# Kernel optimization log

Hardware: AMD Instinct MI355X
Metric: run time of the kernel (lower is better)

## Reference

```python
import jax, jax.numpy as jnp
import numpy as np

NEG_SLOPE = 0.2  # PyG GATConv default leaky_relu slope


def gat_conv(x, src, dst, n, W, a_src, a_dst, bias, concat):
    """PyG-style GATConv (add_self_loops already applied to src/dst)."""
    H, C = a_src.shape
    h = (x @ W).reshape(n, H, C)                      # [N,H,C]
    al_src = jnp.einsum('nhc,hc->nh', h, a_src)       # [N,H]
    al_dst = jnp.einsum('nhc,hc->nh', h, a_dst)       # [N,H]
    e = jax.nn.leaky_relu(al_src[src] + al_dst[dst], NEG_SLOPE)  # [E,H]
    # segment softmax over incoming edges of each dst node
    m = jax.ops.segment_max(e, dst, num_segments=n)   # [N,H]
    ex = jnp.exp(e - m[dst])
    denom = jax.ops.segment_sum(ex, dst, num_segments=n)
    alpha = ex / denom[dst]                            # [E,H]
    out = jax.ops.segment_sum(h[src] * alpha[:, :, None], dst, num_segments=n)  # [N,H,C]
    if concat:
        out = out.reshape(n, H * C)
    else:
        out = out.mean(axis=1)
    return out + bias


def setup_inputs() -> dict:
    key = jax.random.key(0)
    ks = jax.random.split(key, 12)
    N, E = 100000, 1600000
    IN, HID, OUT, H = 128, 16, 32, 4
    x = jax.random.normal(ks[0], (N, IN), dtype=jnp.float32)
    edge_index = jax.random.randint(ks[1], (2, E), 0, N, dtype=jnp.int64)
    s = 0.1
    W1 = jax.random.normal(ks[2], (IN, H * HID), dtype=jnp.float32) * s
    a_src1 = jax.random.normal(ks[3], (H, HID), dtype=jnp.float32) * s
    a_dst1 = jax.random.normal(ks[4], (H, HID), dtype=jnp.float32) * s
    b1 = jnp.zeros((H * HID,), dtype=jnp.float32)
    W2 = jax.random.normal(ks[5], (H * HID, H * OUT), dtype=jnp.float32) * s
    a_src2 = jax.random.normal(ks[6], (H, OUT), dtype=jnp.float32) * s
    a_dst2 = jax.random.normal(ks[7], (H, OUT), dtype=jnp.float32) * s
    b2 = jnp.zeros((OUT,), dtype=jnp.float32)
    return {"x": x, "edge_index": edge_index,
            "W1": W1, "a_src1": a_src1, "a_dst1": a_dst1, "b1": b1,
            "W2": W2, "a_src2": a_src2, "a_dst2": a_dst2, "b2": b2}


def reference(x, edge_index, W1, a_src1, a_dst1, b1, W2, a_src2, a_dst2, b2):
    n = x.shape[0]
    loop = jnp.arange(n, dtype=edge_index.dtype)
    src = jnp.concatenate([edge_index[0], loop])
    dst = jnp.concatenate([edge_index[1], loop])
    # dropout is identity at inference
    h = gat_conv(x, src, dst, n, W1, a_src1, a_dst1, b1, concat=True)
    h = gat_conv(h, src, dst, n, W2, a_src2, a_dst2, b2, concat=False)
    h = jax.nn.elu(h)
    return jax.nn.log_softmax(h, axis=1)
```

## Files before the change

### kernel.cpp

```cpp
#include <hip/hip_runtime.h>
#include <hip/hip_fp16.h>
#include <cstdint>
#include <cstddef>

#define NEG 0.2f
#define TILE 4096


__global__ __launch_bounds__(256) void hist_k(const int* __restrict__ ei, int* __restrict__ cnt, int E) {
    int i = blockIdx.x * 256 + threadIdx.x;
    if (i < E) atomicAdd(&cnt[__builtin_nontemporal_load(ei + E + i)], 1);
}

__global__ __launch_bounds__(256) void scan1_k(const int* __restrict__ cnt, int* __restrict__ rp,
                                               int* __restrict__ bs, int N) {
    __shared__ int sm[256];
    int t = threadIdx.x, i = blockIdx.x * 256 + t;
    int v = (i < N) ? cnt[i] : 0;
    sm[t] = v; __syncthreads();
    for (int off = 1; off < 256; off <<= 1) {
        int u = (t >= off) ? sm[t - off] : 0;
        __syncthreads();
        sm[t] += u;
        __syncthreads();
    }
    if (i < N) rp[i] = sm[t] - v;
    if (t == 255) bs[blockIdx.x] = sm[255];
}

__global__ __launch_bounds__(1024) void scan2_k(int* __restrict__ bs, int nb) {
    __shared__ int sm[1024];
    int t = threadIdx.x;
    int v = (t < nb) ? bs[t] : 0;
    sm[t] = v; __syncthreads();
    for (int off = 1; off < 1024; off <<= 1) {
        int u = (t >= off) ? sm[t - off] : 0;
        __syncthreads();
        sm[t] += u;
        __syncthreads();
    }
    if (t < nb) bs[t] = sm[t] - v;
}

__global__ __launch_bounds__(256) void scan3_k(int* __restrict__ rp, const int* __restrict__ bs, int N) {
    int i = blockIdx.x * 256 + threadIdx.x;
    if (i < N) rp[i] += bs[blockIdx.x];
}

__global__ __launch_bounds__(256) void initA_k(const int* __restrict__ rp, int* __restrict__ curA, int nbk) {
    int b = threadIdx.x;
    if (b < nbk) curA[b] = rp[b << 9];
}


__global__ __launch_bounds__(256) void partA_k(const int* __restrict__ ei, int* __restrict__ curA,
                                               uint2* __restrict__ pairs, int E, int nbk) {
    __shared__ int scnt[256];
    __shared__ int sc[256];
    __shared__ int sbase[256];
    __shared__ int gbase[256];
    __shared__ int cur2[256];
    __shared__ int ssrc[TILE];
    __shared__ int sdst[TILE];
    int t = threadIdx.x;
    int ntiles = (E + TILE - 1) / TILE;
    for (int tile = blockIdx.x; tile < ntiles; tile += gridDim.x) {
        int base = tile * TILE;
        int cntE = min(TILE, E - base);
        scnt[t] = 0;
        __syncthreads();
        int mys[16], myd[16];
        #pragma unroll
        for (int j = 0; j < 16; j++) {
            int i = base + t + 256 * j;
            int s = 0, d = -1;
            if (i < E) {
                s = __builtin_nontemporal_load(ei + i);
                d = __builtin_nontemporal_load(ei + E + i);
            }
            mys[j] = s; myd[j] = d;
            if (d >= 0) atomicAdd(&scnt[d >> 9], 1);
        }
        __syncthreads();
        sc[t] = scnt[t];
        __syncthreads();
        for (int off = 1; off < 256; off <<= 1) {
            int u = (t >= off) ? sc[t - off] : 0;
            __syncthreads();
            sc[t] += u;
            __syncthreads();
        }
        int myb = sc[t] - scnt[t];
        sbase[t] = myb;
        cur2[t] = myb;
        if (t < nbk && scnt[t] > 0) gbase[t] = atomicAdd(&curA[t], scnt[t]);
        __syncthreads();
        #pragma unroll
        for (int j = 0; j < 16; j++) {
            int d = myd[j];
            if (d >= 0) {
                int b = d >> 9;
                int pos = atomicAdd(&cur2[b], 1);
                ssrc[pos] = mys[j];
                sdst[pos] = d;
            }
        }
        __syncthreads();
        for (int i = t; i < cntE; i += 256) {
            int d = sdst[i];
            int b = d >> 9;
            int addr = gbase[b] + (i - sbase[b]);
            pairs[addr] = make_uint2((unsigned)ssrc[i], (unsigned)d);
        }
        __syncthreads();
    }
}


__global__ __launch_bounds__(256) void partB_pairs_k(const uint2* __restrict__ pin, const int* __restrict__ rp,
                                                     int* __restrict__ srcout, int E, int N) {
    __shared__ int cur[512];
    int b = blockIdx.x;
    int t = threadIdx.x;
    int d0 = b << 9;
    cur[t] = 0; cur[t + 256] = 0;
    __syncthreads();
    int hi = d0 + 512;
    int ebase = rp[d0];
    int eend = (hi >= N) ? E : rp[hi];
    for (int j = ebase + t; j < eend; j += 256) {
        uint2 p = pin[j];
        int d = (int)p.y;
        int pos = rp[d] + atomicAdd(&cur[d - d0], 1);
        srcout[pos] = (int)p.x;
    }
}


__global__ __launch_bounds__(256) void gemm1_k(const float* __restrict__ x, const float* __restrict__ W,
                                               const float* __restrict__ a_src, const float* __restrict__ a_dst,
                                               __half* __restrict__ h, float* __restrict__ alsrc,
                                               float* __restrict__ aldst, int N) {
    __shared__ float Bs[128 * 64];
    __shared__ float xs[64][68];
    int t = threadIdx.x;
    for (int i = t; i < 128 * 64 / 4; i += 256)
        ((float4*)Bs)[i] = ((const float4*)W)[i];
    int ct = t & 15, rt = t >> 4;
    int head = ct >> 2, cq = ct & 3;
    float asv[4], adv[4];
    #pragma unroll
    for (int j = 0; j < 4; j++) {
        asv[j] = a_src[head * 16 + 4 * cq + j];
        adv[j] = a_dst[head * 16 + 4 * cq + j];
    }
    int ntiles = (N + 63) >> 6;
    for (int tile = blockIdx.x; tile < ntiles; tile += gridDim.x) {
        int r0 = tile << 6;
        float acc[4][4];
        #pragma unroll
        for (int i = 0; i < 4; i++)
            #pragma unroll
            for (int j = 0; j < 4; j++) acc[i][j] = 0.f;
        for (int kc = 0; kc < 128; kc += 64) {
            __syncthreads();
            int srow = t >> 4, sf4 = t & 15;
            #pragma unroll
            for (int p = 0; p < 4; p++) {
                int r = r0 + srow + 16 * p;
                float4 v = make_float4(0.f, 0.f, 0.f, 0.f);
                if (r < N) v = *(const float4*)(x + (size_t)r * 128 + kc + 4 * sf4);
                *(float4*)&xs[srow + 16 * p][4 * sf4] = v;
            }
            __syncthreads();
            #pragma unroll 4
            for (int k = 0; k < 64; k++) {
                float4 bv = *(float4*)&Bs[(kc + k) * 64 + 4 * ct];
                #pragma unroll
                for (int i = 0; i < 4; i++) {
                    float xv = xs[4 * rt + i][k];
                    acc[i][0] = fmaf(xv, bv.x, acc[i][0]);
                    acc[i][1] = fmaf(xv, bv.y, acc[i][1]);
                    acc[i][2] = fmaf(xv, bv.z, acc[i][2]);
                    acc[i][3] = fmaf(xv, bv.w, acc[i][3]);
                }
            }
        }
        #pragma unroll
        for (int i = 0; i < 4; i++) {
            int r = r0 + 4 * rt + i;
            float ps = 0.f, pd = 0.f;
            #pragma unroll
            for (int j = 0; j < 4; j++) {
                ps = fmaf(acc[i][j], asv[j], ps);
                pd = fmaf(acc[i][j], adv[j], pd);
            }
            ps += __shfl_xor(ps, 1); ps += __shfl_xor(ps, 2);
            pd += __shfl_xor(pd, 1); pd += __shfl_xor(pd, 2);
            if (r < N) {
                __half2 h0 = __floats2half2_rn(acc[i][0], acc[i][1]);
                __half2 h1 = __floats2half2_rn(acc[i][2], acc[i][3]);
                *(__half2*)(h + (size_t)r * 64 + 4 * ct) = h0;
                *(__half2*)(h + (size_t)r * 64 + 4 * ct + 2) = h1;
                if (cq == 0) { alsrc[r * 4 + head] = ps; aldst[r * 4 + head] = pd; }
            }
        }
    }
}


__global__ __launch_bounds__(256) void node1_k(const __half* __restrict__ h, const int* __restrict__ srccol,
                                               const float* __restrict__ alsrc, const float* __restrict__ aldst,
                                               const int* __restrict__ rp, const int* __restrict__ cnt,
                                               const float* __restrict__ bias, __half* __restrict__ out, int N) {
    int t = threadIdx.x;
    int d = (blockIdx.x * 256 + t) >> 4;
    if (d >= N) return;
    int c = t & 15;
    int hc = c >> 2;
    const __half2* hb = (const __half2*)h;
    unsigned co = 2u * c;
    float ad = aldst[d * 4 + hc];
    float e = alsrc[d * 4 + hc] + ad;
    float w = __expf(e > 0.f ? e : NEG * e);
    float den = w;
    __half2 wp = __float2half2_rn(w);
    uint2 u = *(const uint2*)(hb + ((unsigned)d << 5) + co);
    __half2 acc0 = __hmul2(wp, *(__half2*)&u.x);
    __half2 acc1 = __hmul2(wp, *(__half2*)&u.y);
    int start = rp[d], deg = cnt[d];
    int i = 0;
    for (; i + 3 < deg; i += 4) {
        int s0 = srccol[start + i];
        int s1 = srccol[start + i + 1];
        int s2 = srccol[start + i + 2];
        int s3 = srccol[start + i + 3];
        uint2 u0 = *(const uint2*)(hb + ((unsigned)s0 << 5) + co);
        uint2 u1 = *(const uint2*)(hb + ((unsigned)s1 << 5) + co);
        uint2 u2 = *(const uint2*)(hb + ((unsigned)s2 << 5) + co);
        uint2 u3 = *(const uint2*)(hb + ((unsigned)s3 << 5) + co);
        float e0 = alsrc[s0 * 4 + hc] + ad;
        float e1 = alsrc[s1 * 4 + hc] + ad;
        float e2 = alsrc[s2 * 4 + hc] + ad;
        float e3 = alsrc[s3 * 4 + hc] + ad;
        float w0 = __expf(e0 > 0.f ? e0 : NEG * e0);
        float w1 = __expf(e1 > 0.f ? e1 : NEG * e1);
        float w2 = __expf(e2 > 0.f ? e2 : NEG * e2);
        float w3 = __expf(e3 > 0.f ? e3 : NEG * e3);
        den += (w0 + w1) + (w2 + w3);
        __half2 p0 = __float2half2_rn(w0), p1 = __float2half2_rn(w1);
        __half2 p2 = __float2half2_rn(w2), p3 = __float2half2_rn(w3);
        acc0 = __hfma2(p0, *(__half2*)&u0.x, acc0);
        acc1 = __hfma2(p0, *(__half2*)&u0.y, acc1);
        acc0 = __hfma2(p1, *(__half2*)&u1.x, acc0);
        acc1 = __hfma2(p1, *(__half2*)&u1.y, acc1);
        acc0 = __hfma2(p2, *(__half2*)&u2.x, acc0);
        acc1 = __hfma2(p2, *(__half2*)&u2.y, acc1);
        acc0 = __hfma2(p3, *(__half2*)&u3.x, acc0);
        acc1 = __hfma2(p3, *(__half2*)&u3.y, acc1);
    }
    for (; i < deg; i++) {
        int s = srccol[start + i];
        uint2 us = *(const uint2*)(hb + ((unsigned)s << 5) + co);
        float es = alsrc[s * 4 + hc] + ad;
        float ws = __expf(es > 0.f ? es : NEG * es);
        den += ws;
        __half2 wps = __float2half2_rn(ws);
        acc0 = __hfma2(wps, *(__half2*)&us.x, acc0);
        acc1 = __hfma2(wps, *(__half2*)&us.y, acc1);
    }
    float inv = 1.f / den;
    float2 f0 = __half22float2(acc0), f1 = __half22float2(acc1);
    float4 b = *(const float4*)(bias + 4 * c);
    __half2 o0 = __floats2half2_rn(f0.x * inv + b.x, f0.y * inv + b.y);
    __half2 o1 = __floats2half2_rn(f1.x * inv + b.z, f1.y * inv + b.w);
    uint2 o; o.x = *(unsigned*)&o0; o.y = *(unsigned*)&o1;
    *(uint2*)(out + (size_t)d * 64 + 4 * c) = o;
}


__global__ __launch_bounds__(256) void gemm2_k(const __half* __restrict__ xh, const float* __restrict__ W,
                                               const float* __restrict__ a_src, const float* __restrict__ a_dst,
                                               __half* __restrict__ h, float* __restrict__ alsrc,
                                               float* __restrict__ aldst, int N) {
    __shared__ float Bs[64 * 128];
    __shared__ float xs[64][68];
    int t = threadIdx.x;
    for (int i = t; i < 64 * 128 / 4; i += 256)
        ((float4*)Bs)[i] = ((const float4*)W)[i];
    int ct = t & 15, rt = t >> 4;
    int hA = ct >> 3, cq = ct & 7;
    float asA[4], adA[4], asB[4], adB[4];
    #pragma unroll
    for (int j = 0; j < 4; j++) {
        asA[j] = a_src[hA * 32 + 4 * cq + j];
        adA[j] = a_dst[hA * 32 + 4 * cq + j];
        asB[j] = a_src[(2 + hA) * 32 + 4 * cq + j];
        adB[j] = a_dst[(2 + hA) * 32 + 4 * cq + j];
    }
    int ntiles = (N + 63) >> 6;
    for (int tile = blockIdx.x; tile < ntiles; tile += gridDim.x) {
        int r0 = tile << 6;
        float accA[4][4], accB[4][4];
        #pragma unroll
        for (int i = 0; i < 4; i++)
            #pragma unroll
            for (int j = 0; j < 4; j++) { accA[i][j] = 0.f; accB[i][j] = 0.f; }
        __syncthreads();
        int srow = t >> 3, su = t & 7;
        #pragma unroll
        for (int p = 0; p < 2; p++) {
            int r = r0 + srow + 32 * p;
            float2 g0 = make_float2(0.f, 0.f), g1 = g0, g2 = g0, g3 = g0;
            if (r < N) {
                uint4 u = *(const uint4*)(xh + (size_t)r * 64 + 8 * su);
                const __half2* hp = (const __half2*)&u;
                g0 = __half22float2(hp[0]); g1 = __half22float2(hp[1]);
                g2 = __half22float2(hp[2]); g3 = __half22float2(hp[3]);
            }
            *(float4*)&xs[srow + 32 * p][8 * su] = make_float4(g0.x, g0.y, g1.x, g1.y);
            *(float4*)&xs[srow + 32 * p][8 * su + 4] = make_float4(g2.x, g2.y, g3.x, g3.y);
        }
        __syncthreads();
        #pragma unroll 4
        for (int k = 0; k < 64; k++) {
            float4 bA = *(float4*)&Bs[k * 128 + 4 * ct];
            float4 bB = *(float4*)&Bs[k * 128 + 64 + 4 * ct];
            #pragma unroll
            for (int i = 0; i < 4; i++) {
                float xv = xs[4 * rt + i][k];
                accA[i][0] = fmaf(xv, bA.x, accA[i][0]);
                accA[i][1] = fmaf(xv, bA.y, accA[i][1]);
                accA[i][2] = fmaf(xv, bA.z, accA[i][2]);
                accA[i][3] = fmaf(xv, bA.w, accA[i][3]);
                accB[i][0] = fmaf(xv, bB.x, accB[i][0]);
                accB[i][1] = fmaf(xv, bB.y, accB[i][1]);
                accB[i][2] = fmaf(xv, bB.z, accB[i][2]);
                accB[i][3] = fmaf(xv, bB.w, accB[i][3]);
            }
        }
        #pragma unroll
        for (int i = 0; i < 4; i++) {
            int r = r0 + 4 * rt + i;
            float psA = 0.f, pdA = 0.f, psB = 0.f, pdB = 0.f;
            #pragma unroll
            for (int j = 0; j < 4; j++) {
                psA = fmaf(accA[i][j], asA[j], psA);
                pdA = fmaf(accA[i][j], adA[j], pdA);
                psB = fmaf(accB[i][j], asB[j], psB);
                pdB = fmaf(accB[i][j], adB[j], pdB);
            }
            #pragma unroll
            for (int off = 1; off <= 4; off <<= 1) {
                psA += __shfl_xor(psA, off); pdA += __shfl_xor(pdA, off);
                psB += __shfl_xor(psB, off); pdB += __shfl_xor(pdB, off);
            }
            if (r < N) {
                __half2 hA0 = __floats2half2_rn(accA[i][0], accA[i][1]);
                __half2 hA1 = __floats2half2_rn(accA[i][2], accA[i][3]);
                __half2 hB0 = __floats2half2_rn(accB[i][0], accB[i][1]);
                __half2 hB1 = __floats2half2_rn(accB[i][2], accB[i][3]);
                *(__half2*)(h + (size_t)r * 128 + 4 * ct) = hA0;
                *(__half2*)(h + (size_t)r * 128 + 4 * ct + 2) = hA1;
                *(__half2*)(h + (size_t)r * 128 + 64 + 4 * ct) = hB0;
                *(__half2*)(h + (size_t)r * 128 + 64 + 4 * ct + 2) = hB1;
                if (cq == 0) {
                    alsrc[r * 4 + hA] = psA;     alsrc[r * 4 + 2 + hA] = psB;
                    aldst[r * 4 + hA] = pdA;     aldst[r * 4 + 2 + hA] = pdB;
                }
            }
        }
    }
}


__global__ __launch_bounds__(256) void node2_k(const __half* __restrict__ h, const int* __restrict__ srccol,
                                               const float* __restrict__ alsrc, const float* __restrict__ aldst,
                                               const int* __restrict__ rp, const int* __restrict__ cnt,
                                               const float* __restrict__ bias, float* __restrict__ out, int N) {
    int t = threadIdx.x;
    int d = (blockIdx.x * 256 + t) >> 4;
    if (d >= N) return;
    int c = t & 15;
    int hc = c >> 2, jc = c & 3;
    const __half2* hb = (const __half2*)h;
    unsigned co = 4u * c;
    float ad = aldst[d * 4 + hc];
    float e = alsrc[d * 4 + hc] + ad;
    float w = __expf(e > 0.f ? e : NEG * e);
    float den = w;
    __half2 wp = __float2half2_rn(w);
    uint4 u = *(const uint4*)(hb + ((unsigned)d << 6) + co);
    const __half2* hp = (const __half2*)&u;
    __half2 acc[4];
    #pragma unroll
    for (int j = 0; j < 4; j++) acc[j] = __hmul2(wp, hp[j]);
    int start = rp[d], deg = cnt[d];
    int i = 0;
    for (; i + 3 < deg; i += 4) {
        int s0 = srccol[start + i];
        int s1 = srccol[start + i + 1];
        int s2 = srccol[start + i + 2];
        int s3 = srccol[start + i + 3];
        uint4 u0 = *(const uint4*)(hb + ((unsigned)s0 << 6) + co);
        uint4 u1 = *(const uint4*)(hb + ((unsigned)s1 << 6) + co);
        uint4 u2 = *(const uint4*)(hb + ((unsigned)s2 << 6) + co);
        uint4 u3 = *(const uint4*)(hb + ((unsigned)s3 << 6) + co);
        float e0 = alsrc[s0 * 4 + hc] + ad;
        float e1 = alsrc[s1 * 4 + hc] + ad;
        float e2 = alsrc[s2 * 4 + hc] + ad;
        float e3 = alsrc[s3 * 4 + hc] + ad;
        float w0 = __expf(e0 > 0.f ? e0 : NEG * e0);
        float w1 = __expf(e1 > 0.f ? e1 : NEG * e1);
        float w2 = __expf(e2 > 0.f ? e2 : NEG * e2);
        float w3 = __expf(e3 > 0.f ? e3 : NEG * e3);
        den += (w0 + w1) + (w2 + w3);
        __half2 p0 = __float2half2_rn(w0), p1 = __float2half2_rn(w1);
        __half2 p2 = __float2half2_rn(w2), p3 = __float2half2_rn(w3);
        const __half2* q0 = (const __half2*)&u0;
        const __half2* q1 = (const __half2*)&u1;
        const __half2* q2 = (const __half2*)&u2;
        const __half2* q3 = (const __half2*)&u3;
        #pragma unroll
        for (int j = 0; j < 4; j++) acc[j] = __hfma2(p0, q0[j], acc[j]);
        #pragma unroll
        for (int j = 0; j < 4; j++) acc[j] = __hfma2(p1, q1[j], acc[j]);
        #pragma unroll
        for (int j = 0; j < 4; j++) acc[j] = __hfma2(p2, q2[j], acc[j]);
        #pragma unroll
        for (int j = 0; j < 4; j++) acc[j] = __hfma2(p3, q3[j], acc[j]);
    }
    for (; i < deg; i++) {
        int s = srccol[start + i];
        uint4 us = *(const uint4*)(hb + ((unsigned)s << 6) + co);
        float es = alsrc[s * 4 + hc] + ad;
        float ws = __expf(es > 0.f ? es : NEG * es);
        den += ws;
        __half2 wps = __float2half2_rn(ws);
        const __half2* hps = (const __half2*)&us;
        #pragma unroll
        for (int j = 0; j < 4; j++) acc[j] = __hfma2(wps, hps[j], acc[j]);
    }
    float inv = 1.f / den;
    float v[8];
    #pragma unroll
    for (int j = 0; j < 4; j++) {
        float2 f = __half22float2(acc[j]);
        v[2 * j] = f.x * inv; v[2 * j + 1] = f.y * inv;
    }
    #pragma unroll
    for (int off = 4; off <= 8; off <<= 1) {
        #pragma unroll
        for (int j = 0; j < 8; j++) v[j] += __shfl_xor(v[j], off);
    }
    float ev[8];
    #pragma unroll
    for (int j = 0; j < 8; j++) {
        float val = 0.25f * v[j] + bias[8 * jc + j];
        ev[j] = val > 0.f ? val : __expf(val) - 1.f;
    }
    float mx = ev[0];
    #pragma unroll
    for (int j = 1; j < 8; j++) mx = fmaxf(mx, ev[j]);
    #pragma unroll
    for (int off = 1; off <= 2; off <<= 1) mx = fmaxf(mx, __shfl_xor(mx, off));
    float sum = 0.f;
    #pragma unroll
    for (int j = 0; j < 8; j++) sum += __expf(ev[j] - mx);
    #pragma unroll
    for (int off = 1; off <= 2; off <<= 1) sum += __shfl_xor(sum, off);
    float ls = mx + __logf(sum);
    if (c < 4) {
        float4 o0, o1;
        o0.x = ev[0] - ls; o0.y = ev[1] - ls; o0.z = ev[2] - ls; o0.w = ev[3] - ls;
        o1.x = ev[4] - ls; o1.y = ev[5] - ls; o1.z = ev[6] - ls; o1.w = ev[7] - ls;
        *(float4*)(out + (size_t)d * 32 + 8 * jc) = o0;
        *(float4*)(out + (size_t)d * 32 + 8 * jc + 4) = o1;
    }
}


extern "C" void kernel_launch(void* const* d_in, const int* in_sizes, int n_in,
                              void* d_out, int out_size, void* d_ws, size_t ws_size,
                              hipStream_t stream) {
    const float* x   = (const float*)d_in[0];
    const int*   ei  = (const int*)d_in[1];
    const float* W1  = (const float*)d_in[2];
    const float* as1 = (const float*)d_in[3];
    const float* ad1 = (const float*)d_in[4];
    const float* b1  = (const float*)d_in[5];
    const float* W2  = (const float*)d_in[6];
    const float* as2 = (const float*)d_in[7];
    const float* ad2 = (const float*)d_in[8];
    const float* b2  = (const float*)d_in[9];
    float* out = (float*)d_out;
    int N = in_sizes[0] / 128;
    int E = in_sizes[1] / 2;

    char* base = (char*)d_ws;
    size_t off = 0;
    auto alloc = [&](size_t bytes) -> char* {
        char* p = base + off;
        off = (off + bytes + 255) & ~(size_t)255;
        return p;
    };
    __half* h1h   = (__half*)alloc((size_t)N * 64 * 2);
    __half* h1o   = (__half*)alloc((size_t)N * 64 * 2);
    __half* h2h   = (__half*)alloc((size_t)N * 128 * 2);
    float* alsrc1 = (float*)alloc((size_t)N * 4 * 4);
    float* aldst1 = (float*)alloc((size_t)N * 4 * 4);
    float* alsrc2 = (float*)alloc((size_t)N * 4 * 4);
    float* aldst2 = (float*)alloc((size_t)N * 4 * 4);
    int* cnt  = (int*)alloc((size_t)N * 4);
    int* rp   = (int*)alloc((size_t)N * 4);
    int* curA = (int*)alloc(256 * 4);
    int* bs   = (int*)alloc(1024 * 4);
    int* srccol = (int*)alloc((size_t)E * 4);
    uint2* pairs = (uint2*)alloc((size_t)E * 8);

    int nbk = (N + 511) >> 9;
    int ntilesA = (E + TILE - 1) / TILE;
    int nb = (N + 255) / 256;

    hipMemsetAsync(cnt, 0, (size_t)N * 4, stream);
    hist_k<<<(E + 255) / 256, 256, 0, stream>>>(ei, cnt, E);
    scan1_k<<<nb, 256, 0, stream>>>(cnt, rp, bs, N);
    scan2_k<<<1, 1024, 0, stream>>>(bs, nb);
    scan3_k<<<nb, 256, 0, stream>>>(rp, bs, N);
    initA_k<<<1, 256, 0, stream>>>(rp, curA, nbk);
    partA_k<<<ntilesA, 256, 0, stream>>>(ei, curA, pairs, E, nbk);
    partB_pairs_k<<<nbk, 256, 0, stream>>>(pairs, rp, srccol, E, N);

    gemm1_k<<<768, 256, 0, stream>>>(x, W1, as1, ad1, h1h, alsrc1, aldst1, N);
    node1_k<<<(N + 15) / 16, 256, 0, stream>>>(h1h, srccol, alsrc1, aldst1, rp, cnt, b1, h1o, N);
    gemm2_k<<<768, 256, 0, stream>>>(h1o, W2, as2, ad2, h2h, alsrc2, aldst2, N);
    node2_k<<<(N + 15) / 16, 256, 0, stream>>>(h2h, srccol, alsrc2, aldst2, rp, cnt, b2, out, N);
}
```

Before: 384.9 us.

## Reorder layer-2 GAT to aggregate before projection using precomputed attention vectors

Layer 2 now folds the attention vectors into W2 (W2·a_src and W2·a_dst, precomputed in a small kernel), so the attention logits come straight from the 64-wide layer-1 output. The edge gather then reads the 64-wide h1o instead of the 128-wide projected features. It keeps per-head aggregates in a 256-wide fp16 buffer, and a final GEMM applies W2 per head, adds the bias and fuses the head mean, ELU and log_softmax. The goal is to halve gather traffic in the edge-heavy aggregation, at the cost of a larger intermediate write and read and a bigger GEMM. That intermediate buffer reuses the workspace that previously held h1h and pairs.

```diff
diff --git a/kernel.cpp b/kernel.cpp
--- a/kernel.cpp
+++ b/kernel.cpp
@@ -279,122 +279,94 @@
 }
 
 
-__global__ __launch_bounds__(256) void gemm2_k(const __half* __restrict__ xh, const float* __restrict__ W,
-                                               const float* __restrict__ a_src, const float* __restrict__ a_dst,
-                                               __half* __restrict__ h, float* __restrict__ alsrc,
-                                               float* __restrict__ aldst, int N) {
-    __shared__ float Bs[64 * 128];
-    __shared__ float xs[64][68];
-    int t = threadIdx.x;
-    for (int i = t; i < 64 * 128 / 4; i += 256)
-        ((float4*)Bs)[i] = ((const float4*)W)[i];
-    int ct = t & 15, rt = t >> 4;
-    int hA = ct >> 3, cq = ct & 7;
-    float asA[4], adA[4], asB[4], adB[4];
-    #pragma unroll
-    for (int j = 0; j < 4; j++) {
-        asA[j] = a_src[hA * 32 + 4 * cq + j];
-        adA[j] = a_dst[hA * 32 + 4 * cq + j];
-        asB[j] = a_src[(2 + hA) * 32 + 4 * cq + j];
-        adB[j] = a_dst[(2 + hA) * 32 + 4 * cq + j];
-    }
-    int ntiles = (N + 63) >> 6;
-    for (int tile = blockIdx.x; tile < ntiles; tile += gridDim.x) {
-        int r0 = tile << 6;
-        float accA[4][4], accB[4][4];
-        #pragma unroll
-        for (int i = 0; i < 4; i++)
-            #pragma unroll
-            for (int j = 0; j < 4; j++) { accA[i][j] = 0.f; accB[i][j] = 0.f; }
-        __syncthreads();
-        int srow = t >> 3, su = t & 7;
-        #pragma unroll
-        for (int p = 0; p < 2; p++) {
-            int r = r0 + srow + 32 * p;
-            float2 g0 = make_float2(0.f, 0.f), g1 = g0, g2 = g0, g3 = g0;
-            if (r < N) {
-                uint4 u = *(const uint4*)(xh + (size_t)r * 64 + 8 * su);
-                const __half2* hp = (const __half2*)&u;
-                g0 = __half22float2(hp[0]); g1 = __half22float2(hp[1]);
-                g2 = __half22float2(hp[2]); g3 = __half22float2(hp[3]);
-            }
-            *(float4*)&xs[srow + 32 * p][8 * su] = make_float4(g0.x, g0.y, g1.x, g1.y);
-            *(float4*)&xs[srow + 32 * p][8 * su + 4] = make_float4(g2.x, g2.y, g3.x, g3.y);
-        }
-        __syncthreads();
-        #pragma unroll 4
-        for (int k = 0; k < 64; k++) {
-            float4 bA = *(float4*)&Bs[k * 128 + 4 * ct];
-            float4 bB = *(float4*)&Bs[k * 128 + 64 + 4 * ct];
-            #pragma unroll
-            for (int i = 0; i < 4; i++) {
-                float xv = xs[4 * rt + i][k];
-                accA[i][0] = fmaf(xv, bA.x, accA[i][0]);
-                accA[i][1] = fmaf(xv, bA.y, accA[i][1]);
-                accA[i][2] = fmaf(xv, bA.z, accA[i][2]);
-                accA[i][3] = fmaf(xv, bA.w, accA[i][3]);
-                accB[i][0] = fmaf(xv, bB.x, accB[i][0]);
-                accB[i][1] = fmaf(xv, bB.y, accB[i][1]);
-                accB[i][2] = fmaf(xv, bB.z, accB[i][2]);
-                accB[i][3] = fmaf(xv, bB.w, accB[i][3]);
-            }
-        }
-        #pragma unroll
-        for (int i = 0; i < 4; i++) {
-            int r = r0 + 4 * rt + i;
-            float psA = 0.f, pdA = 0.f, psB = 0.f, pdB = 0.f;
-            #pragma unroll
-            for (int j = 0; j < 4; j++) {
-                psA = fmaf(accA[i][j], asA[j], psA);
-                pdA = fmaf(accA[i][j], adA[j], pdA);
-                psB = fmaf(accB[i][j], asB[j], psB);
-                pdB = fmaf(accB[i][j], adB[j], pdB);
-            }
-            #pragma unroll
-            for (int off = 1; off <= 4; off <<= 1) {
-                psA += __shfl_xor(psA, off); pdA += __shfl_xor(pdA, off);
-                psB += __shfl_xor(psB, off); pdB += __shfl_xor(pdB, off);
-            }
-            if (r < N) {
-                __half2 hA0 = __floats2half2_rn(accA[i][0], accA[i][1]);
-                __half2 hA1 = __floats2half2_rn(accA[i][2], accA[i][3]);
-                __half2 hB0 = __floats2half2_rn(accB[i][0], accB[i][1]);
-                __half2 hB1 = __floats2half2_rn(accB[i][2], accB[i][3]);
-                *(__half2*)(h + (size_t)r * 128 + 4 * ct) = hA0;
-                *(__half2*)(h + (size_t)r * 128 + 4 * ct + 2) = hA1;
-                *(__half2*)(h + (size_t)r * 128 + 64 + 4 * ct) = hB0;
-                *(__half2*)(h + (size_t)r * 128 + 64 + 4 * ct + 2) = hB1;
-                if (cq == 0) {
-                    alsrc[r * 4 + hA] = psA;     alsrc[r * 4 + 2 + hA] = psB;
-                    aldst[r * 4 + hA] = pdA;     aldst[r * 4 + 2 + hA] = pdB;
-                }
-            }
-        }
-    }
-}
-
-
-__global__ __launch_bounds__(256) void node2_k(const __half* __restrict__ h, const int* __restrict__ srccol,
-                                               const float* __restrict__ alsrc, const float* __restrict__ aldst,
-                                               const int* __restrict__ rp, const int* __restrict__ cnt,
-                                               const float* __restrict__ bias, float* __restrict__ out, int N) {
+__global__ __launch_bounds__(256) void prew_k(const float* __restrict__ W2, const float* __restrict__ as2,
+                                              const float* __restrict__ ad2, float* __restrict__ was,
+                                              float* __restrict__ wad) {
+    int t = threadIdx.x;
+    int k = t >> 2, hh = t & 3;
+    const float* wrow = W2 + k * 128 + hh * 32;
+    const float* av = as2 + hh * 32;
+    const float* dv = ad2 + hh * 32;
+    float s = 0.f, ds = 0.f;
+    #pragma unroll 8
+    for (int c = 0; c < 32; c++) {
+        float w = wrow[c];
+        s = fmaf(w, av[c], s);
+        ds = fmaf(w, dv[c], ds);
+    }
+    was[t] = s;
+    wad[t] = ds;
+}
+
+
+__global__ __launch_bounds__(256) void alv2_k(const __half* __restrict__ h1o, const float* __restrict__ was,
+                                              const float* __restrict__ wad, float* __restrict__ alsrc,
+                                              float* __restrict__ aldst, int N) {
     int t = threadIdx.x;
     int d = (blockIdx.x * 256 + t) >> 4;
     if (d >= N) return;
     int c = t & 15;
-    int hc = c >> 2, jc = c & 3;
-    const __half2* hb = (const __half2*)h;
-    unsigned co = 4u * c;
-    float ad = aldst[d * 4 + hc];
-    float e = alsrc[d * 4 + hc] + ad;
+    uint2 u = *(const uint2*)(h1o + (size_t)d * 64 + 4 * c);
+    float2 f0 = __half22float2(*(__half2*)&u.x);
+    float2 f1 = __half22float2(*(__half2*)&u.y);
+    float v0 = f0.x, v1 = f0.y, v2 = f1.x, v3 = f1.y;
+    const float4* was4 = (const float4*)was;
+    const float4* wad4 = (const float4*)wad;
+    float4 wa0 = was4[4 * c + 0], wa1 = was4[4 * c + 1], wa2 = was4[4 * c + 2], wa3 = was4[4 * c + 3];
+    float4 wd0 = wad4[4 * c + 0], wd1 = wad4[4 * c + 1], wd2 = wad4[4 * c + 2], wd3 = wad4[4 * c + 3];
+    float4 ps, pd;
+    ps.x = fmaf(v0, wa0.x, fmaf(v1, wa1.x, fmaf(v2, wa2.x, v3 * wa3.x)));
+    ps.y = fmaf(v0, wa0.y, fmaf(v1, wa1.y, fmaf(v2, wa2.y, v3 * wa3.y)));
+    ps.z = fmaf(v0, wa0.z, fmaf(v1, wa1.z, fmaf(v2, wa2.z, v3 * wa3.z)));
+    ps.w = fmaf(v0, wa0.w, fmaf(v1, wa1.w, fmaf(v2, wa2.w, v3 * wa3.w)));
+    pd.x = fmaf(v0, wd0.x, fmaf(v1, wd1.x, fmaf(v2, wd2.x, v3 * wd3.x)));
+    pd.y = fmaf(v0, wd0.y, fmaf(v1, wd1.y, fmaf(v2, wd2.y, v3 * wd3.y)));
+    pd.z = fmaf(v0, wd0.z, fmaf(v1, wd1.z, fmaf(v2, wd2.z, v3 * wd3.z)));
+    pd.w = fmaf(v0, wd0.w, fmaf(v1, wd1.w, fmaf(v2, wd2.w, v3 * wd3.w)));
+    #pragma unroll
+    for (int off = 1; off <= 8; off <<= 1) {
+        ps.x += __shfl_xor(ps.x, off); ps.y += __shfl_xor(ps.y, off);
+        ps.z += __shfl_xor(ps.z, off); ps.w += __shfl_xor(ps.w, off);
+        pd.x += __shfl_xor(pd.x, off); pd.y += __shfl_xor(pd.y, off);
+        pd.z += __shfl_xor(pd.z, off); pd.w += __shfl_xor(pd.w, off);
+    }
+    if (c == 0) {
+        *(float4*)(alsrc + (size_t)d * 4) = ps;
+        *(float4*)(aldst + (size_t)d * 4) = pd;
+    }
+}
+
+
+#define ACC8(P, A, B) { const __half2* qa = (const __half2*)&(A); const __half2* qb = (const __half2*)&(B); \
+    acc0 = __hfma2(P, qa[0], acc0); acc1 = __hfma2(P, qa[1], acc1); \
+    acc2 = __hfma2(P, qa[2], acc2); acc3 = __hfma2(P, qa[3], acc3); \
+    acc4 = __hfma2(P, qb[0], acc4); acc5 = __hfma2(P, qb[1], acc5); \
+    acc6 = __hfma2(P, qb[2], acc6); acc7 = __hfma2(P, qb[3], acc7); }
+
+__global__ __launch_bounds__(256) void node2_k(const __half* __restrict__ h1o, const int* __restrict__ srccol,
+                                               const float* __restrict__ alsrc, const float* __restrict__ aldst,
+                                               const int* __restrict__ rp, const int* __restrict__ cnt,
+                                               __half* __restrict__ y, int N) {
+    int t = threadIdx.x;
+    int d = (blockIdx.x * 256 + t) >> 4;
+    if (d >= N) return;
+    int c = t & 15;
+    int h = c >> 2;
+    unsigned co = 2u * (unsigned)(c & 3);
+    const uint4* hb = (const uint4*)h1o;
+    float ad = aldst[d * 4 + h];
+    float e = alsrc[d * 4 + h] + ad;
     float w = __expf(e > 0.f ? e : NEG * e);
     float den = w;
     __half2 wp = __float2half2_rn(w);
-    uint4 u = *(const uint4*)(hb + ((unsigned)d << 6) + co);
-    const __half2* hp = (const __half2*)&u;
-    __half2 acc[4];
-    #pragma unroll
-    for (int j = 0; j < 4; j++) acc[j] = __hmul2(wp, hp[j]);
+    uint4 ua = hb[((unsigned)d << 3) + co];
+    uint4 ub = hb[((unsigned)d << 3) + co + 1];
+    const __half2* pa = (const __half2*)&ua;
+    const __half2* pb = (const __half2*)&ub;
+    __half2 acc0 = __hmul2(wp, pa[0]), acc1 = __hmul2(wp, pa[1]);
+    __half2 acc2 = __hmul2(wp, pa[2]), acc3 = __hmul2(wp, pa[3]);
+    __half2 acc4 = __hmul2(wp, pb[0]), acc5 = __hmul2(wp, pb[1]);
+    __half2 acc6 = __hmul2(wp, pb[2]), acc7 = __hmul2(wp, pb[3]);
     int start = rp[d], deg = cnt[d];
     int i = 0;
     for (; i + 3 < deg; i += 4) {
@@ -402,14 +374,14 @@
         int s1 = srccol[start + i + 1];
         int s2 = srccol[start + i + 2];
         int s3 = srccol[start + i + 3];
-        uint4 u0 = *(const uint4*)(hb + ((unsigned)s0 << 6) + co);
-        uint4 u1 = *(const uint4*)(hb + ((unsigned)s1 << 6) + co);
-        uint4 u2 = *(const uint4*)(hb + ((unsigned)s2 << 6) + co);
-        uint4 u3 = *(const uint4*)(hb + ((unsigned)s3 << 6) + co);
-        float e0 = alsrc[s0 * 4 + hc] + ad;
-        float e1 = alsrc[s1 * 4 + hc] + ad;
-        float e2 = alsrc[s2 * 4 + hc] + ad;
-        float e3 = alsrc[s3 * 4 + hc] + ad;
+        uint4 a0 = hb[((unsigned)s0 << 3) + co], b0 = hb[((unsigned)s0 << 3) + co + 1];
+        uint4 a1 = hb[((unsigned)s1 << 3) + co], b1 = hb[((unsigned)s1 << 3) + co + 1];
+        uint4 a2 = hb[((unsigned)s2 << 3) + co], b2 = hb[((unsigned)s2 << 3) + co + 1];
+        uint4 a3 = hb[((unsigned)s3 << 3) + co], b3 = hb[((unsigned)s3 << 3) + co + 1];
+        float e0 = alsrc[s0 * 4 + h] + ad;
+        float e1 = alsrc[s1 * 4 + h] + ad;
+        float e2 = alsrc[s2 * 4 + h] + ad;
+        float e3 = alsrc[s3 * 4 + h] + ad;
         float w0 = __expf(e0 > 0.f ? e0 : NEG * e0);
         float w1 = __expf(e1 > 0.f ? e1 : NEG * e1);
         float w2 = __expf(e2 > 0.f ? e2 : NEG * e2);
@@ -417,65 +389,109 @@
         den += (w0 + w1) + (w2 + w3);
         __half2 p0 = __float2half2_rn(w0), p1 = __float2half2_rn(w1);
         __half2 p2 = __float2half2_rn(w2), p3 = __float2half2_rn(w3);
-        const __half2* q0 = (const __half2*)&u0;
-        const __half2* q1 = (const __half2*)&u1;
-        const __half2* q2 = (const __half2*)&u2;
-        const __half2* q3 = (const __half2*)&u3;
-        #pragma unroll
-        for (int j = 0; j < 4; j++) acc[j] = __hfma2(p0, q0[j], acc[j]);
-        #pragma unroll
-        for (int j = 0; j < 4; j++) acc[j] = __hfma2(p1, q1[j], acc[j]);
-        #pragma unroll
-        for (int j = 0; j < 4; j++) acc[j] = __hfma2(p2, q2[j], acc[j]);
-        #pragma unroll
-        for (int j = 0; j < 4; j++) acc[j] = __hfma2(p3, q3[j], acc[j]);
+        ACC8(p0, a0, b0)
+        ACC8(p1, a1, b1)
+        ACC8(p2, a2, b2)
+        ACC8(p3, a3, b3)
     }
     for (; i < deg; i++) {
         int s = srccol[start + i];
-        uint4 us = *(const uint4*)(hb + ((unsigned)s << 6) + co);
-        float es = alsrc[s * 4 + hc] + ad;
+        uint4 as = hb[((unsigned)s << 3) + co], bs = hb[((unsigned)s << 3) + co + 1];
+        float es = alsrc[s * 4 + h] + ad;
         float ws = __expf(es > 0.f ? es : NEG * es);
         den += ws;
-        __half2 wps = __float2half2_rn(ws);
-        const __half2* hps = (const __half2*)&us;
+        __half2 pws = __float2half2_rn(ws);
+        ACC8(pws, as, bs)
+    }
+    float inv = 0.25f / den;
+    __half2 ip = __float2half2_rn(inv);
+    uint4 oA, oB;
+    __half2* oa = (__half2*)&oA; __half2* ob = (__half2*)&oB;
+    oa[0] = __hmul2(ip, acc0); oa[1] = __hmul2(ip, acc1);
+    oa[2] = __hmul2(ip, acc2); oa[3] = __hmul2(ip, acc3);
+    ob[0] = __hmul2(ip, acc4); ob[1] = __hmul2(ip, acc5);
+    ob[2] = __hmul2(ip, acc6); ob[3] = __hmul2(ip, acc7);
+    __half* yp = y + (size_t)d * 256 + 16u * (unsigned)c;
+    *(uint4*)yp = oA;
+    *(uint4*)(yp + 8) = oB;
+}
+
+
+__global__ __launch_bounds__(256) void gemm3_k(const __half* __restrict__ y, const float* __restrict__ W2,
+                                               const float* __restrict__ bias, float* __restrict__ out, int N) {
+    __shared__ __half2 ws[256 * 16];
+    __shared__ __half2 ys[64 * 134];
+    int t = threadIdx.x;
+    for (int i = t; i < 4096; i += 256) {
+        int kp = i >> 4, c2 = i & 15;
+        int hh = kp >> 6, kk = kp & 63;
+        const float* wp = W2 + kk * 128 + hh * 32 + 2 * c2;
+        ws[i] = __floats2half2_rn(wp[0], wp[1]);
+    }
+    int ct = t & 7, rt = t >> 3;
+    float4 b4 = *(const float4*)(bias + 4 * ct);
+    int ntiles = (N + 63) >> 6;
+    for (int tile = blockIdx.x; tile < ntiles; tile += gridDim.x) {
+        int r0 = tile << 6;
+        __syncthreads();
+        for (int i = t; i < 64 * 64; i += 256) {
+            int row = i >> 6, k4 = i & 63;
+            uint2 v = make_uint2(0u, 0u);
+            int r = r0 + row;
+            if (r < N) v = *(const uint2*)(y + (size_t)r * 256 + 4 * k4);
+            *(uint2*)&ys[row * 134 + 2 * k4] = v;
+        }
+        __syncthreads();
+        float acc[2][4];
         #pragma unroll
-        for (int j = 0; j < 4; j++) acc[j] = __hfma2(wps, hps[j], acc[j]);
-    }
-    float inv = 1.f / den;
-    float v[8];
-    #pragma unroll
-    for (int j = 0; j < 4; j++) {
-        float2 f = __half22float2(acc[j]);
-        v[2 * j] = f.x * inv; v[2 * j + 1] = f.y * inv;
-    }
-    #pragma unroll
-    for (int off = 4; off <= 8; off <<= 1) {
+        for (int r = 0; r < 2; r++)
+            #pragma unroll
+            for (int j = 0; j < 4; j++) acc[r][j] = 0.f;
+        const __half2* yr0 = ys + (2 * rt) * 134;
+        const __half2* yr1 = ys + (2 * rt + 1) * 134;
+        #pragma unroll 4
+        for (int k2 = 0; k2 < 128; k2++) {
+            const __half2* wk0 = ws + (2 * k2) * 16;
+            const __half2* wk1 = wk0 + 16;
+            float2 wA0 = __half22float2(wk0[2 * ct]);
+            float2 wA1 = __half22float2(wk0[2 * ct + 1]);
+            float2 wB0 = __half22float2(wk1[2 * ct]);
+            float2 wB1 = __half22float2(wk1[2 * ct + 1]);
+            float2 xa = __half22float2(yr0[k2]);
+            float2 xb = __half22float2(yr1[k2]);
+            acc[0][0] = fmaf(xa.x, wA0.x, acc[0][0]); acc[0][1] = fmaf(xa.x, wA0.y, acc[0][1]);
+            acc[0][2] = fmaf(xa.x, wA1.x, acc[0][2]); acc[0][3] = fmaf(xa.x, wA1.y, acc[0][3]);
+            acc[0][0] = fmaf(xa.y, wB0.x, acc[0][0]); acc[0][1] = fmaf(xa.y, wB0.y, acc[0][1]);
+            acc[0][2] = fmaf(xa.y, wB1.x, acc[0][2]); acc[0][3] = fmaf(xa.y, wB1.y, acc[0][3]);
+            acc[1][0] = fmaf(xb.x, wA0.x, acc[1][0]); acc[1][1] = fmaf(xb.x, wA0.y, acc[1][1]);
+            acc[1][2] = fmaf(xb.x, wA1.x, acc[1][2]); acc[1][3] = fmaf(xb.x, wA1.y, acc[1][3]);
+            acc[1][0] = fmaf(xb.y, wB0.x, acc[1][0]); acc[1][1] = fmaf(xb.y, wB0.y, acc[1][1]);
+            acc[1][2] = fmaf(xb.y, wB1.x, acc[1][2]); acc[1][3] = fmaf(xb.y, wB1.y, acc[1][3]);
+        }
         #pragma unroll
-        for (int j = 0; j < 8; j++) v[j] += __shfl_xor(v[j], off);
-    }
-    float ev[8];
-    #pragma unroll
-    for (int j = 0; j < 8; j++) {
-        float val = 0.25f * v[j] + bias[8 * jc + j];
-        ev[j] = val > 0.f ? val : __expf(val) - 1.f;
-    }
-    float mx = ev[0];
-    #pragma unroll
-    for (int j = 1; j < 8; j++) mx = fmaxf(mx, ev[j]);
-    #pragma unroll
-    for (int off = 1; off <= 2; off <<= 1) mx = fmaxf(mx, __shfl_xor(mx, off));
-    float sum = 0.f;
-    #pragma unroll
-    for (int j = 0; j < 8; j++) sum += __expf(ev[j] - mx);
-    #pragma unroll
-    for (int off = 1; off <= 2; off <<= 1) sum += __shfl_xor(sum, off);
-    float ls = mx + __logf(sum);
-    if (c < 4) {
-        float4 o0, o1;
-        o0.x = ev[0] - ls; o0.y = ev[1] - ls; o0.z = ev[2] - ls; o0.w = ev[3] - ls;
-        o1.x = ev[4] - ls; o1.y = ev[5] - ls; o1.z = ev[6] - ls; o1.w = ev[7] - ls;
-        *(float4*)(out + (size_t)d * 32 + 8 * jc) = o0;
-        *(float4*)(out + (size_t)d * 32 + 8 * jc + 4) = o1;
+        for (int r = 0; r < 2; r++) {
+            int row = r0 + 2 * rt + r;
+            float ev0 = acc[r][0] + b4.x;
+            float ev1 = acc[r][1] + b4.y;
+            float ev2 = acc[r][2] + b4.z;
+            float ev3 = acc[r][3] + b4.w;
+            ev0 = ev0 > 0.f ? ev0 : __expf(ev0) - 1.f;
+            ev1 = ev1 > 0.f ? ev1 : __expf(ev1) - 1.f;
+            ev2 = ev2 > 0.f ? ev2 : __expf(ev2) - 1.f;
+            ev3 = ev3 > 0.f ? ev3 : __expf(ev3) - 1.f;
+            float mx = fmaxf(fmaxf(ev0, ev1), fmaxf(ev2, ev3));
+            #pragma unroll
+            for (int off = 1; off <= 4; off <<= 1) mx = fmaxf(mx, __shfl_xor(mx, off));
+            float sm = __expf(ev0 - mx) + __expf(ev1 - mx) + __expf(ev2 - mx) + __expf(ev3 - mx);
+            #pragma unroll
+            for (int off = 1; off <= 4; off <<= 1) sm += __shfl_xor(sm, off);
+            float ls = mx + __logf(sm);
+            if (row < N) {
+                float4 o;
+                o.x = ev0 - ls; o.y = ev1 - ls; o.z = ev2 - ls; o.w = ev3 - ls;
+                *(float4*)(out + (size_t)row * 32 + 4 * ct) = o;
+            }
+        }
     }
 }
 
@@ -504,24 +520,27 @@
         off = (off + bytes + 255) & ~(size_t)255;
         return p;
     };
-    __half* h1h   = (__half*)alloc((size_t)N * 64 * 2);
+    __half* y     = (__half*)alloc((size_t)N * 256 * 2);
+    __half* h1h   = (__half*)y;
+    uint2*  pairs = (uint2*)((char*)y + (size_t)N * 64 * 2);
     __half* h1o   = (__half*)alloc((size_t)N * 64 * 2);
-    __half* h2h   = (__half*)alloc((size_t)N * 128 * 2);
     float* alsrc1 = (float*)alloc((size_t)N * 4 * 4);
     float* aldst1 = (float*)alloc((size_t)N * 4 * 4);
     float* alsrc2 = (float*)alloc((size_t)N * 4 * 4);
     float* aldst2 = (float*)alloc((size_t)N * 4 * 4);
+    float* was    = (float*)alloc(256 * 4);
+    float* wad    = (float*)alloc(256 * 4);
     int* cnt  = (int*)alloc((size_t)N * 4);
     int* rp   = (int*)alloc((size_t)N * 4);
     int* curA = (int*)alloc(256 * 4);
     int* bs   = (int*)alloc(1024 * 4);
     int* srccol = (int*)alloc((size_t)E * 4);
-    uint2* pairs = (uint2*)alloc((size_t)E * 8);
 
     int nbk = (N + 511) >> 9;
     int ntilesA = (E + TILE - 1) / TILE;
     int nb = (N + 255) / 256;
 
+    prew_k<<<1, 256, 0, stream>>>(W2, as2, ad2, was, wad);
     hipMemsetAsync(cnt, 0, (size_t)N * 4, stream);
     hist_k<<<(E + 255) / 256, 256, 0, stream>>>(ei, cnt, E);
     scan1_k<<<nb, 256, 0, stream>>>(cnt, rp, bs, N);
@@ -533,6 +552,7 @@
 
     gemm1_k<<<768, 256, 0, stream>>>(x, W1, as1, ad1, h1h, alsrc1, aldst1, N);
     node1_k<<<(N + 15) / 16, 256, 0, stream>>>(h1h, srccol, alsrc1, aldst1, rp, cnt, b1, h1o, N);
-    gemm2_k<<<768, 256, 0, stream>>>(h1o, W2, as2, ad2, h2h, alsrc2, aldst2, N);
-    node2_k<<<(N + 15) / 16, 256, 0, stream>>>(h2h, srccol, alsrc2, aldst2, rp, cnt, b2, out, N);
-}
+    alv2_k<<<(N + 15) / 16, 256, 0, stream>>>(h1o, was, wad, alsrc2, aldst2, N);
+    node2_k<<<(N + 15) / 16, 256, 0, stream>>>(h1o, srccol, alsrc2, aldst2, rp, cnt, y, N);
+    gemm3_k<<<768, 256, 0, stream>>>(y, W2, b2, out, N);
+}
```

Result: slower. 413.7 us (+7.5%).
